# Optimization experiments

Measured on AMD Instinct MI355X. Metric: run time of the kernel, lower is better.

## Reference

```python
import jax, jax.numpy as jnp
import numpy as np

E = 1024   # embed_dim
H = 16     # num_heads
D = E // H # head_dim
B = 2
S = 2048
YAT_EPS = 0.1


def setup_inputs() -> dict:
    key = jax.random.key(0)
    ks = jax.random.split(key, 5)
    w_scale = (6.0 / (E + E)) ** 0.5  # xavier_uniform bound
    def xavier(k):
        return jax.random.uniform(k, (E, E), jnp.float32, -w_scale, w_scale)
    return {
        "x": jax.random.normal(ks[0], (B, S, E), jnp.float32),
        "Wq": xavier(ks[1]), "bq": jnp.zeros((E,), jnp.float32),
        "Wk": xavier(ks[2]), "bk": jnp.zeros((E,), jnp.float32),
        "Wv": xavier(ks[3]), "bv": jnp.zeros((E,), jnp.float32),
        "Wo": xavier(ks[4]), "bo": jnp.zeros((E,), jnp.float32),
    }


def reference(x, Wq, bq, Wk, bk, Wv, bv, Wo, bo):
    b, s, _ = x.shape
    # Projections (Linear: x @ W + b, flax kernel layout [in, out])
    Q = x @ Wq + bq
    K = x @ Wk + bk
    V = x @ Wv + bv
    # [B, H, S, D]
    Q = Q.reshape(b, s, H, D).transpose(0, 2, 1, 3)
    K = K.reshape(b, s, H, D).transpose(0, 2, 1, 3)
    V = V.reshape(b, s, H, D).transpose(0, 2, 1, 3)
    # L2 normalize along head_dim
    Qn = Q / (jnp.linalg.norm(Q, axis=-1, keepdims=True) + 1e-8)
    Kn = K / (jnp.linalg.norm(K, axis=-1, keepdims=True) + 1e-8)
    # Yat kernel scores: (1 + <q,k>)^2 / (eps + (1 - <q,k>))
    dot = jnp.einsum("bhqd,bhkd->bhqk", Qn, Kn)
    scores = (1.0 + dot) ** 2 / (YAT_EPS + (1.0 - dot))
    # Sum-normalize (no softmax)
    attn = scores / (jnp.sum(scores, axis=-1, keepdims=True) + 1e-6)
    out = jnp.einsum("bhqk,bhkd->bhqd", attn, V)
    out = out.transpose(0, 2, 1, 3).reshape(b, s, E)
    return out @ Wo + bo
```

## Files before the change

kernel.cpp:

```cpp
#include <hip/hip_runtime.h>
#include <math.h>

#define EDIM 1024
#define NH   16
#define HD   64
#define BATCH 2
#define SEQ  2048
#define NROW (BATCH*SEQ)
#define YAT_EPS 0.1f

typedef _Float16 f16;
typedef _Float16 f16x8 __attribute__((ext_vector_type(8)));
typedef _Float16 f16x4 __attribute__((ext_vector_type(4)));
typedef float    f32x4 __attribute__((ext_vector_type(4)));

#define GLL16(gp, lp) __builtin_amdgcn_global_load_lds( \
    (const __attribute__((address_space(1))) void*)(gp), \
    (__attribute__((address_space(3))) void*)(lp), 16, 0, 0)

__global__ __launch_bounds__(256)
void cast_f16_kernel(const float* __restrict__ src, f16* __restrict__ dst)
{
    const int i = (blockIdx.x * 256 + threadIdx.x) * 4;
    const float4 v = *(const float4*)(src + i);
    f16x4 o = {(f16)v.x, (f16)v.y, (f16)v.z, (f16)v.w};
    *(f16x4*)(dst + i) = o;
}

__global__ __launch_bounds__(256)
void transcast4_kernel(const float* __restrict__ W0, const float* __restrict__ W1,
                       const float* __restrict__ W2, const float* __restrict__ W3,
                       f16* __restrict__ T0, f16* __restrict__ T1,
                       f16* __restrict__ T2, f16* __restrict__ T3)
{
    const int z = blockIdx.z;
    const float* W = (z == 0) ? W0 : (z == 1) ? W1 : (z == 2) ? W2 : W3;
    f16*         Wt = (z == 0) ? T0 : (z == 1) ? T1 : (z == 2) ? T2 : T3;

    __shared__ float T[32][33];
    const int t = threadIdx.x;
    const int r = t >> 3, c4 = (t & 7) * 4;
    const int bi = blockIdx.x * 32, bj = blockIdx.y * 32;
    const float4 v = *(const float4*)(W + (size_t)(bi + r) * 1024 + bj + c4);
    T[r][c4 + 0] = v.x; T[r][c4 + 1] = v.y; T[r][c4 + 2] = v.z; T[r][c4 + 3] = v.w;
    __syncthreads();
    f16x4 o = {(f16)T[c4 + 0][r], (f16)T[c4 + 1][r], (f16)T[c4 + 2][r], (f16)T[c4 + 3][r]};
    *(f16x4*)(Wt + (size_t)(bj + r) * 1024 + bi + c4) = o;
}

template<int BM>
__global__ __launch_bounds__(256)
void gemm_f16(const f16* __restrict__ A,
              const f16* __restrict__ B0, const f16* __restrict__ B1, const f16* __restrict__ B2,
              const float* __restrict__ bi0, const float* __restrict__ bi1, const float* __restrict__ bi2,
              void* __restrict__ o0, void* __restrict__ o1, void* __restrict__ o2,
              int e0, int e1, int e2)
{
    constexpr int MT   = BM / 32;
    constexpr int LA   = BM / 64;
    constexpr int ABUF = BM * 32;
    constexpr int BBUF = 128 * 32;
    constexpr int STG  = 2 * (ABUF + BBUF) * 2;
    constexpr int EPI  = BM * 128 * 2;
    constexpr int LDSB = STG > EPI ? STG : EPI;
    __shared__ __align__(16) char lds[LDSB];
    f16* As = (f16*)lds;
    f16* Bs = (f16*)lds + 2 * ABUF;

    const int z = blockIdx.z;
    const f16*   Bt   = (z == 0) ? B0  : (z == 1) ? B1  : B2;
    const float* bias = (z == 0) ? bi0 : (z == 1) ? bi1 : bi2;
    void*        Cout = (z == 0) ? o0  : (z == 1) ? o1  : o2;
    const int    epi  = (z == 0) ? e0  : (z == 1) ? e1  : e2;

    const int tid  = threadIdx.x;
    const int lane = tid & 63;
    const int w    = tid >> 6;
    const int cl   = lane & 15;
    const int quad = lane >> 4;
    const int wm = w & 1, wn = w >> 1;
    const int bm = blockIdx.x * BM, bn = blockIdx.y * 128;
    const int wmoff = wm * (MT * 16);

    const int srow = tid >> 2;
    const int sc   = tid & 3;
    const int ssw  = (sc ^ (srow & 3)) * 8;
    const f16* gA = A  + (size_t)(bm + srow) * 1024 + sc * 8;
    const f16* gB = Bt + (size_t)(bn + srow) * 1024 + sc * 8;
    int lAo[LA], lBo[2];
#pragma unroll
    for (int i = 0; i < LA; ++i) lAo[i] = (srow + i * 64) * 32 + ssw;
#pragma unroll
    for (int i = 0; i < 2;  ++i) lBo[i] = (srow + i * 64) * 32 + ssw;

    f32x4 acc[MT][4];
#pragma unroll
    for (int i = 0; i < MT; ++i)
#pragma unroll
        for (int j = 0; j < 4; ++j) acc[i][j] = (f32x4){0.f, 0.f, 0.f, 0.f};

    f16x8 ra[LA], rb[2];

#pragma unroll
    for (int i = 0; i < LA; ++i) ra[i] = *(const f16x8*)(gA + (size_t)i * 64 * 1024);
#pragma unroll
    for (int i = 0; i < 2;  ++i) rb[i] = *(const f16x8*)(gB + (size_t)i * 64 * 1024);
#pragma unroll
    for (int i = 0; i < LA; ++i) *(f16x8*)(As + lAo[i]) = ra[i];
#pragma unroll
    for (int i = 0; i < 2;  ++i) *(f16x8*)(Bs + lBo[i]) = rb[i];
#pragma unroll
    for (int i = 0; i < LA; ++i) ra[i] = *(const f16x8*)(gA + (size_t)i * 64 * 1024 + 32);
#pragma unroll
    for (int i = 0; i < 2;  ++i) rb[i] = *(const f16x8*)(gB + (size_t)i * 64 * 1024 + 32);
    __syncthreads();

    const int fsw = (quad ^ (cl & 3)) * 8;

    for (int it = 0; it < 32; ++it) {
        const int buf = it & 1, nb = buf ^ 1;
        if (it < 31) {
#pragma unroll
            for (int i = 0; i < LA; ++i) *(f16x8*)(As + nb * ABUF + lAo[i]) = ra[i];
#pragma unroll
            for (int i = 0; i < 2;  ++i) *(f16x8*)(Bs + nb * BBUF + lBo[i]) = rb[i];
        }
        if (it < 30) {
            const int kn = (it + 2) * 32;
#pragma unroll
            for (int i = 0; i < LA; ++i) ra[i] = *(const f16x8*)(gA + (size_t)i * 64 * 1024 + kn);
#pragma unroll
            for (int i = 0; i < 2;  ++i) rb[i] = *(const f16x8*)(gB + (size_t)i * 64 * 1024 + kn);
        }
        f16x8 af[MT], bf[4];
#pragma unroll
        for (int mt = 0; mt < MT; ++mt)
            af[mt] = *(const f16x8*)(&As[buf * ABUF + (wmoff + mt * 16 + cl) * 32 + fsw]);
#pragma unroll
        for (int nt = 0; nt < 4; ++nt)
            bf[nt] = *(const f16x8*)(&Bs[buf * BBUF + (wn * 64 + nt * 16 + cl) * 32 + fsw]);
#pragma unroll
        for (int mt = 0; mt < MT; ++mt)
#pragma unroll
            for (int nt = 0; nt < 4; ++nt)
                acc[mt][nt] = __builtin_amdgcn_mfma_f32_16x16x32_f16(af[mt], bf[nt], acc[mt][nt], 0, 0, 0);
        __syncthreads();
    }

    float bcol[4];
#pragma unroll
    for (int nt = 0; nt < 4; ++nt) bcol[nt] = bias[bn + wn * 64 + nt * 16 + cl];
#pragma unroll
    for (int mt = 0; mt < MT; ++mt)
#pragma unroll
        for (int nt = 0; nt < 4; ++nt)
#pragma unroll
            for (int rg = 0; rg < 4; ++rg) acc[mt][nt][rg] += bcol[nt];

    const int b_idx = bm >> 11, sl0 = bm & (SEQ - 1), h0 = bn >> 6;

    if (epi == 0) {
        float* C = (float*)Cout;
#pragma unroll
        for (int mt = 0; mt < MT; ++mt)
#pragma unroll
            for (int rg = 0; rg < 4; ++rg) {
                const int row = bm + wmoff + mt * 16 + quad * 4 + rg;
#pragma unroll
                for (int nt = 0; nt < 4; ++nt)
                    C[(size_t)row * EDIM + bn + wn * 64 + nt * 16 + cl] = acc[mt][nt][rg];
            }
    } else if (epi == 1) {
        f16* C = (f16*)Cout;
        __syncthreads();
        f16* S = (f16*)lds;
#pragma unroll
        for (int mt = 0; mt < MT; ++mt)
#pragma unroll
            for (int rg = 0; rg < 4; ++rg) {
                float ss = 0.f;
#pragma unroll
                for (int nt = 0; nt < 4; ++nt) ss += acc[mt][nt][rg] * acc[mt][nt][rg];
                ss += __shfl_xor(ss, 1); ss += __shfl_xor(ss, 2);
                ss += __shfl_xor(ss, 4); ss += __shfl_xor(ss, 8);
                const float inv = 1.0f / (sqrtf(ss) + 1e-8f);
                const int row = wmoff + mt * 16 + quad * 4 + rg;
#pragma unroll
                for (int nt = 0; nt < 4; ++nt) {
                    const int col = wn * 64 + nt * 16 + cl;
                    S[row * 128 + (((col >> 3) ^ (row & 15)) * 8) + (col & 7)] =
                        (f16)(acc[mt][nt][rg] * inv);
                }
            }
        __syncthreads();
#pragma unroll
        for (int i = 0; i < BM / 16; ++i) {
            const int c = tid + i * 256;
            const int s = c >> 4, gi = c & 15;
            f16x8 v = *(const f16x8*)(&S[s * 128 + ((gi ^ (s & 15)) * 8)]);
            const int head = h0 + (gi >> 3), d8 = (gi & 7) * 8;
            *(f16x8*)(C + ((size_t)(b_idx * NH + head) * SEQ + sl0 + s) * HD + d8) = v;
        }
    } else {
        f16* C = (f16*)Cout;
        __syncthreads();
        f16* S = (f16*)lds;
        constexpr int GM = BM / 8 - 1;
#pragma unroll
        for (int mt = 0; mt < MT; ++mt) {
            const int s0 = wmoff + mt * 16 + quad * 4;
#pragma unroll
            for (int nt = 0; nt < 4; ++nt) {
                const int col = wn * 64 + nt * 16 + cl;
                f16x4 o = {(f16)acc[mt][nt][0], (f16)acc[mt][nt][1],
                           (f16)acc[mt][nt][2], (f16)acc[mt][nt][3]};
                *(f16x4*)(&S[col * BM + (((s0 >> 3) ^ (col & GM)) * 8) + (s0 & 7)]) = o;
            }
        }
        __syncthreads();
        constexpr int GSH = (BM == 128) ? 4 : 3;
#pragma unroll
        for (int i = 0; i < BM / 16; ++i) {
            const int c = tid + i * 256;
            const int col = c >> GSH, gi = c & GM;
            f16x8 v = *(const f16x8*)(&S[col * BM + ((gi ^ (col & GM)) * 8)]);
            const int head = h0 + (col >> 6), d = col & 63;
            *(f16x8*)(C + ((size_t)(b_idx * NH + head) * HD + d) * SEQ + sl0 + gi * 8) = v;
        }
    }
}

__global__ __launch_bounds__(256)
void yat_attn(const f16* __restrict__ Qh, const f16* __restrict__ Kh,
              const f16* __restrict__ Vt, f16* __restrict__ AO)
{
    __shared__ __align__(16) char lds[53248];
    f16* KsB = (f16*)(lds + 20480);
    f16* VsB = (f16*)(lds + 36864);

    const int tid  = threadIdx.x;
    const int lane = tid & 63;
    const int w    = tid >> 6;
    const int cl   = lane & 15;
    const int quad = lane >> 4;
    const int wm = w & 1;
    const int wk = w >> 1;
    const int q0 = blockIdx.x * 128;
    const int bh = blockIdx.y;

    const f16* Qg = Qh + (size_t)bh * SEQ * HD;
    const f16* Kg = Kh + (size_t)bh * SEQ * HD;
    const f16* Vg = Vt + (size_t)bh * HD * SEQ;

    const int g8   = lane >> 3;
    const int scs  = (lane & 7) ^ g8;
    const int qrow = w * 8 + g8;
    const int krow = w * 16 + g8;

    {
        const f16* gQ = Qg + (size_t)(q0 + qrow) * HD + scs * 8;
        f16* lQ = (f16*)lds + w * 512;
#pragma unroll
        for (int it = 0; it < 4; ++it)
            GLL16(gQ + it * 32 * HD, lQ + it * 2048);
    }
    __syncthreads();
    f16x8 qf[4][2];
#pragma unroll
    for (int qt = 0; qt < 4; ++qt)
#pragma unroll
        for (int kb = 0; kb < 2; ++kb)
            qf[qt][kb] = *(const f16x8*)((f16*)lds + (wm * 64 + qt * 16 + cl) * 64 +
                                         ((kb * 4 + quad) ^ (cl & 7)) * 8);
    __syncthreads();

    f16* Pw = (f16*)(lds + w * 5120);

    f32x4 O[4][4];
    float rs[4] = {0.f, 0.f, 0.f, 0.f};
#pragma unroll
    for (int i = 0; i < 4; ++i)
#pragma unroll
        for (int j = 0; j < 4; ++j) O[i][j] = (f32x4){0.f, 0.f, 0.f, 0.f};

    const f16* gK = Kg + (size_t)krow * HD + scs * 8;
    const f16* gV = Vg + (size_t)krow * SEQ + scs * 8;
    f16* lK = KsB + w * 1024;
    f16* lV = VsB + w * 1024;

#pragma unroll
    for (int it = 0; it < 2; ++it) {
        GLL16(gK + (size_t)(it * 8) * HD, lK + it * 512);
        GLL16(gV + (size_t)(it * 8) * SEQ, lV + it * 512);
    }

    for (int t0 = 0; t0 < SEQ; t0 += 64) {
        const int buf = (t0 >> 6) & 1;
        __syncthreads();

        if (t0 + 64 < SEQ) {
            const int nb = buf ^ 1;
#pragma unroll
            for (int it = 0; it < 2; ++it) {
                GLL16(gK + (size_t)(t0 + 64 + it * 8) * HD, lK + nb * 4096 + it * 512);
                GLL16(gV + (size_t)(it * 8) * SEQ + t0 + 64, lV + nb * 4096 + it * 512);
            }
        }

        const f16* Ks = KsB + buf * 4096;
        const f16* Vs = VsB + buf * 4096;

        f32x4 s[2][4];
#pragma unroll
        for (int kt = 0; kt < 2; ++kt)
#pragma unroll
            for (int qt = 0; qt < 4; ++qt) s[kt][qt] = (f32x4){0.f, 0.f, 0.f, 0.f};
#pragma unroll
        for (int kb = 0; kb < 2; ++kb) {
            const int sw = ((kb * 4 + quad) ^ (cl & 7)) * 8;
            f16x8 af0 = *(const f16x8*)(&Ks[(wk * 32 +  0 + cl) * 64 + sw]);
            f16x8 af1 = *(const f16x8*)(&Ks[(wk * 32 + 16 + cl) * 64 + sw]);
#pragma unroll
            for (int qt = 0; qt < 4; ++qt) {
                s[0][qt] = __builtin_amdgcn_mfma_f32_16x16x32_f16(af0, qf[qt][kb], s[0][qt], 0, 0, 0);
                s[1][qt] = __builtin_amdgcn_mfma_f32_16x16x32_f16(af1, qf[qt][kb], s[1][qt], 0, 0, 0);
            }
        }

#pragma unroll
        for (int kt = 0; kt < 2; ++kt)
#pragma unroll
            for (int qt = 0; qt < 4; ++qt) {
                f16x4 pk;
                float psum = 0.f;
#pragma unroll
                for (int rg = 0; rg < 4; ++rg) {
                    const float u = (1.0f + YAT_EPS) - s[kt][qt][rg];
                    const float p = fmaf(4.41f, __builtin_amdgcn_rcpf(u), u - 4.2f);
                    psum += p;
                    pk[rg] = (f16)p;
                }
                rs[qt] += psum;
                *(f16x4*)(&Pw[(qt * 16 + cl) * 40 + kt * 16 + quad * 4]) = pk;
            }

        f16x8 pa[4];
#pragma unroll
        for (int qt = 0; qt < 4; ++qt)
            pa[qt] = *(const f16x8*)(&Pw[(qt * 16 + cl) * 40 + quad * 8]);
#pragma unroll
        for (int dn = 0; dn < 4; ++dn) {
            f16x8 vb = *(const f16x8*)(&Vs[(dn * 16 + cl) * 64 +
                                           ((wk * 4 + quad) ^ (cl & 7)) * 8]);
#pragma unroll
            for (int qt = 0; qt < 4; ++qt)
                O[qt][dn] = __builtin_amdgcn_mfma_f32_16x16x32_f16(pa[qt], vb, O[qt][dn], 0, 0, 0);
        }
    }

    __syncthreads();
    float* rs_s = (float*)lds;
    float* Ox   = (float*)(lds + 20480);

#pragma unroll
    for (int qt = 0; qt < 4; ++qt) {
        float t = rs[qt];
        t += __shfl_xor(t, 16);
        t += __shfl_xor(t, 32);
        if (quad == 0) rs_s[wk * 128 + wm * 64 + qt * 16 + cl] = t;
    }
    if (wk == 1) {
#pragma unroll
        for (int qt = 0; qt < 4; ++qt)
#pragma unroll
            for (int dn = 0; dn < 4; ++dn)
#pragma unroll
                for (int rg = 0; rg < 4; ++rg)
                    Ox[(wm * 64 + qt * 16 + quad * 4 + rg) * 64 + dn * 16 + cl] = O[qt][dn][rg];
    }
    __syncthreads();
    if (wk == 0) {
        const int b = bh >> 4, h = bh & 15;
#pragma unroll
        for (int qt = 0; qt < 4; ++qt)
#pragma unroll
            for (int rg = 0; rg < 4; ++rg) {
                const int ql = wm * 64 + qt * 16 + quad * 4 + rg;
                const float tot = rs_s[ql] + rs_s[128 + ql];
                const float inv = 1.0f / (tot + 1e-6f);
                const size_t rowoff = ((size_t)b * SEQ + q0 + ql) * EDIM + h * 64;
#pragma unroll
                for (int dn = 0; dn < 4; ++dn)
                    AO[rowoff + dn * 16 + cl] =
                        (f16)((O[qt][dn][rg] + Ox[ql * 64 + dn * 16 + cl]) * inv);
            }
    }
}

extern "C" void kernel_launch(void* const* d_in, const int* in_sizes, int n_in,
                              void* d_out, int out_size, void* d_ws, size_t ws_size,
                              hipStream_t stream)
{
    const float* x  = (const float*)d_in[0];
    const float* Wq = (const float*)d_in[1];
    const float* bq = (const float*)d_in[2];
    const float* Wk = (const float*)d_in[3];
    const float* bk = (const float*)d_in[4];
    const float* Wv = (const float*)d_in[5];
    const float* bv = (const float*)d_in[6];
    const float* Wo = (const float*)d_in[7];
    const float* bo = (const float*)d_in[8];

    char* p = (char*)d_ws;
    f16* xb  = (f16*)p;                 p += (size_t)NROW * EDIM * 2;
    f16* Wqt = (f16*)p;                 p += (size_t)EDIM * EDIM * 2;
    f16* Wkt = (f16*)p;                 p += (size_t)EDIM * EDIM * 2;
    f16* Wvt = (f16*)p;                 p += (size_t)EDIM * EDIM * 2;
    f16* Wot = (f16*)p;                 p += (size_t)EDIM * EDIM * 2;
    f16* Qhb = (f16*)p;                 p += (size_t)NROW * EDIM * 2;
    f16* Khb = (f16*)p;                 p += (size_t)NROW * EDIM * 2;
    f16* Vtb = (f16*)p;                 p += (size_t)NROW * EDIM * 2;
    f16* AOb = (f16*)p;                 p += (size_t)NROW * EDIM * 2;

    cast_f16_kernel<<<NROW * EDIM / 1024, 256, 0, stream>>>(x, xb);
    transcast4_kernel<<<dim3(32, 32, 4), 256, 0, stream>>>(Wq, Wk, Wv, Wo,
                                                           Wqt, Wkt, Wvt, Wot);

    gemm_f16<128><<<dim3(NROW / 128, EDIM / 128, 3), 256, 0, stream>>>(
        xb, Wqt, Wkt, Wvt, bq, bk, bv, Qhb, Khb, Vtb, 1, 1, 2);

    yat_attn<<<dim3(SEQ / 128, BATCH * NH), 256, 0, stream>>>(Qhb, Khb, Vtb, AOb);

    gemm_f16<64><<<dim3(NROW / 64, EDIM / 128, 1), 256, 0, stream>>>(
        AOb, Wot, Wot, Wot, bo, bo, bo, d_out, d_out, d_out, 0, 0, 0);
}
```

Before: 209.2 us.

## Fuse x cast into QKV GEMM and restructure attention to 512 threads

Measured after the change: 205.6 us. No clear change (-1.7%).

```diff
diff --git a/kernel.cpp b/kernel.cpp
--- a/kernel.cpp
+++ b/kernel.cpp
@@ -12,19 +12,21 @@
 typedef _Float16 f16;
 typedef _Float16 f16x8 __attribute__((ext_vector_type(8)));
 typedef _Float16 f16x4 __attribute__((ext_vector_type(4)));
+typedef __fp16   h16x2 __attribute__((ext_vector_type(2)));
 typedef float    f32x4 __attribute__((ext_vector_type(4)));
 
-#define GLL16(gp, lp) __builtin_amdgcn_global_load_lds( \
-    (const __attribute__((address_space(1))) void*)(gp), \
-    (__attribute__((address_space(3))) void*)(lp), 16, 0, 0)
-
-__global__ __launch_bounds__(256)
-void cast_f16_kernel(const float* __restrict__ src, f16* __restrict__ dst)
-{
-    const int i = (blockIdx.x * 256 + threadIdx.x) * 4;
-    const float4 v = *(const float4*)(src + i);
-    f16x4 o = {(f16)v.x, (f16)v.y, (f16)v.z, (f16)v.w};
-    *(f16x4*)(dst + i) = o;
+static __device__ __forceinline__ int pk2(float a, float b) {
+    union { h16x2 h; int i; } u;
+    u.h = __builtin_amdgcn_cvt_pkrtz(a, b);
+    return u.i;
+}
+static __device__ __forceinline__ f16x8 cvt_f16x8(float4 a, float4 b) {
+    union { int i[4]; f16x8 h; } u;
+    u.i[0] = pk2(a.x, a.y);
+    u.i[1] = pk2(a.z, a.w);
+    u.i[2] = pk2(b.x, b.y);
+    u.i[3] = pk2(b.z, b.w);
+    return u.h;
 }
 
 __global__ __launch_bounds__(256)
@@ -48,9 +50,9 @@
     *(f16x4*)(Wt + (size_t)(bj + r) * 1024 + bi + c4) = o;
 }
 
-template<int BM>
+template<int BM, bool AF32>
 __global__ __launch_bounds__(256)
-void gemm_f16(const f16* __restrict__ A,
+void gemm_f16(const void* __restrict__ Av,
               const f16* __restrict__ B0, const f16* __restrict__ B1, const f16* __restrict__ B2,
               const float* __restrict__ bi0, const float* __restrict__ bi1, const float* __restrict__ bi2,
               void* __restrict__ o0, void* __restrict__ o1, void* __restrict__ o2,
@@ -85,8 +87,9 @@
     const int srow = tid >> 2;
     const int sc   = tid & 3;
     const int ssw  = (sc ^ (srow & 3)) * 8;
-    const f16* gA = A  + (size_t)(bm + srow) * 1024 + sc * 8;
-    const f16* gB = Bt + (size_t)(bn + srow) * 1024 + sc * 8;
+    const float* gAf = (const float*)Av + (size_t)(bm + srow) * 1024 + sc * 8;
+    const f16*   gAh = (const f16*)Av   + (size_t)(bm + srow) * 1024 + sc * 8;
+    const f16*   gB  = Bt + (size_t)(bn + srow) * 1024 + sc * 8;
     int lAo[LA], lBo[2];
 #pragma unroll
     for (int i = 0; i < LA; ++i) lAo[i] = (srow + i * 64) * 32 + ssw;
@@ -101,8 +104,12 @@
 
     f16x8 ra[LA], rb[2];
 
-#pragma unroll
-    for (int i = 0; i < LA; ++i) ra[i] = *(const f16x8*)(gA + (size_t)i * 64 * 1024);
+#define LOAD_A(i, kn) (AF32 ? cvt_f16x8(*(const float4*)(gAf + (size_t)(i) * 64 * 1024 + (kn)),      \
+                                        *(const float4*)(gAf + (size_t)(i) * 64 * 1024 + (kn) + 4))  \
+                            : *(const f16x8*)(gAh + (size_t)(i) * 64 * 1024 + (kn)))
+
+#pragma unroll
+    for (int i = 0; i < LA; ++i) ra[i] = LOAD_A(i, 0);
 #pragma unroll
     for (int i = 0; i < 2;  ++i) rb[i] = *(const f16x8*)(gB + (size_t)i * 64 * 1024);
 #pragma unroll
@@ -110,7 +117,7 @@
 #pragma unroll
     for (int i = 0; i < 2;  ++i) *(f16x8*)(Bs + lBo[i]) = rb[i];
 #pragma unroll
-    for (int i = 0; i < LA; ++i) ra[i] = *(const f16x8*)(gA + (size_t)i * 64 * 1024 + 32);
+    for (int i = 0; i < LA; ++i) ra[i] = LOAD_A(i, 32);
 #pragma unroll
     for (int i = 0; i < 2;  ++i) rb[i] = *(const f16x8*)(gB + (size_t)i * 64 * 1024 + 32);
     __syncthreads();
@@ -128,7 +135,7 @@
         if (it < 30) {
             const int kn = (it + 2) * 32;
 #pragma unroll
-            for (int i = 0; i < LA; ++i) ra[i] = *(const f16x8*)(gA + (size_t)i * 64 * 1024 + kn);
+            for (int i = 0; i < LA; ++i) ra[i] = LOAD_A(i, kn);
 #pragma unroll
             for (int i = 0; i < 2;  ++i) rb[i] = *(const f16x8*)(gB + (size_t)i * 64 * 1024 + kn);
         }
@@ -146,6 +153,7 @@
                 acc[mt][nt] = __builtin_amdgcn_mfma_f32_16x16x32_f16(af[mt], bf[nt], acc[mt][nt], 0, 0, 0);
         __syncthreads();
     }
+#undef LOAD_A
 
     float bcol[4];
 #pragma unroll
@@ -230,21 +238,22 @@
     }
 }
 
-__global__ __launch_bounds__(256)
+__global__ __launch_bounds__(512, 4)
 void yat_attn(const f16* __restrict__ Qh, const f16* __restrict__ Kh,
               const f16* __restrict__ Vt, f16* __restrict__ AO)
 {
-    __shared__ __align__(16) char lds[53248];
-    f16* KsB = (f16*)(lds + 20480);
-    f16* VsB = (f16*)(lds + 36864);
+    __shared__ __align__(16) char lds[49152];
+    f16* Qs = (f16*)lds;
+    f16* KB = (f16*)(lds + 16384);
+    f16* VB = (f16*)(lds + 32768);
 
     const int tid  = threadIdx.x;
     const int lane = tid & 63;
     const int w    = tid >> 6;
     const int cl   = lane & 15;
     const int quad = lane >> 4;
-    const int wm = w & 1;
-    const int wk = w >> 1;
+    const int wm = w & 3;
+    const int wk = w >> 2;
     const int q0 = blockIdx.x * 128;
     const int bh = blockIdx.y;
 
@@ -252,140 +261,141 @@
     const f16* Kg = Kh + (size_t)bh * SEQ * HD;
     const f16* Vg = Vt + (size_t)bh * HD * SEQ;
 
-    const int g8   = lane >> 3;
-    const int scs  = (lane & 7) ^ g8;
-    const int qrow = w * 8 + g8;
-    const int krow = w * 16 + g8;
-
-    {
-        const f16* gQ = Qg + (size_t)(q0 + qrow) * HD + scs * 8;
-        f16* lQ = (f16*)lds + w * 512;
-#pragma unroll
-        for (int it = 0; it < 4; ++it)
-            GLL16(gQ + it * 32 * HD, lQ + it * 2048);
+    const int rkv = tid >> 3;
+    const int gkv = tid & 7;
+    const f16* gK = Kg + (size_t)rkv * HD + gkv * 8;
+    const f16* gV = Vg + (size_t)rkv * SEQ + gkv * 8;
+    const int lkOff = rkv * 64 + ((gkv ^ (rkv & 7)) * 8);
+
+    f16x8 kr = *(const f16x8*)(gK);
+    f16x8 vr = *(const f16x8*)(gV);
+
+#pragma unroll
+    for (int i = 0; i < 2; ++i) {
+        const int s0 = tid + i * 512;
+        const int row = s0 >> 3, g = s0 & 7;
+        f16x8 v = *(const f16x8*)(Qg + (size_t)(q0 + row) * HD + g * 8);
+        *(f16x8*)(&Qs[row * 64 + ((g ^ (row & 7)) * 8)]) = v;
     }
     __syncthreads();
-    f16x8 qf[4][2];
-#pragma unroll
-    for (int qt = 0; qt < 4; ++qt)
+    f16x8 qf[2][2];
+#pragma unroll
+    for (int qt = 0; qt < 2; ++qt)
 #pragma unroll
         for (int kb = 0; kb < 2; ++kb)
-            qf[qt][kb] = *(const f16x8*)((f16*)lds + (wm * 64 + qt * 16 + cl) * 64 +
-                                         ((kb * 4 + quad) ^ (cl & 7)) * 8);
-    __syncthreads();
-
-    f16* Pw = (f16*)(lds + w * 5120);
-
-    f32x4 O[4][4];
-    float rs[4] = {0.f, 0.f, 0.f, 0.f};
-#pragma unroll
-    for (int i = 0; i < 4; ++i)
+            qf[qt][kb] = *(const f16x8*)(&Qs[(wm * 32 + qt * 16 + cl) * 64 +
+                                             ((kb * 4 + quad) ^ (cl & 7)) * 8]);
+
+    f32x4 O[2][4];
+    float rs[2] = {0.f, 0.f};
+#pragma unroll
+    for (int i = 0; i < 2; ++i)
 #pragma unroll
         for (int j = 0; j < 4; ++j) O[i][j] = (f32x4){0.f, 0.f, 0.f, 0.f};
 
-    const f16* gK = Kg + (size_t)krow * HD + scs * 8;
-    const f16* gV = Vg + (size_t)krow * SEQ + scs * 8;
-    f16* lK = KsB + w * 1024;
-    f16* lV = VsB + w * 1024;
-
-#pragma unroll
-    for (int it = 0; it < 2; ++it) {
-        GLL16(gK + (size_t)(it * 8) * HD, lK + it * 512);
-        GLL16(gV + (size_t)(it * 8) * SEQ, lV + it * 512);
-    }
-
-    for (int t0 = 0; t0 < SEQ; t0 += 64) {
-        const int buf = (t0 >> 6) & 1;
-        __syncthreads();
-
-        if (t0 + 64 < SEQ) {
-            const int nb = buf ^ 1;
-#pragma unroll
-            for (int it = 0; it < 2; ++it) {
-                GLL16(gK + (size_t)(t0 + 64 + it * 8) * HD, lK + nb * 4096 + it * 512);
-                GLL16(gV + (size_t)(it * 8) * SEQ + t0 + 64, lV + nb * 4096 + it * 512);
-            }
-        }
-
-        const f16* Ks = KsB + buf * 4096;
-        const f16* Vs = VsB + buf * 4096;
-
-        f32x4 s[2][4];
+    const int addrA = ((((quad & 1) << 1) * 16) + cl) << 2;
+    const int addrB = addrA + 64;
+
+    for (int t = 0; t < 32; ++t) {
+        const int buf = t & 1;
+        *(f16x8*)(&KB[buf * 4096 + lkOff]) = kr;
+        *(f16x8*)(&VB[buf * 4096 + lkOff]) = vr;
+        if (t < 31) {
+            kr = *(const f16x8*)(gK + (size_t)(t + 1) * 64 * HD);
+            vr = *(const f16x8*)(gV + (t + 1) * 64);
+        }
+        __syncthreads();
+
+        const f16* Ks = KB + buf * 4096;
+        const f16* Vs = VB + buf * 4096;
+
+        f32x4 s[2][2];
 #pragma unroll
         for (int kt = 0; kt < 2; ++kt)
 #pragma unroll
-            for (int qt = 0; qt < 4; ++qt) s[kt][qt] = (f32x4){0.f, 0.f, 0.f, 0.f};
+            for (int qt = 0; qt < 2; ++qt) s[kt][qt] = (f32x4){0.f, 0.f, 0.f, 0.f};
 #pragma unroll
         for (int kb = 0; kb < 2; ++kb) {
             const int sw = ((kb * 4 + quad) ^ (cl & 7)) * 8;
             f16x8 af0 = *(const f16x8*)(&Ks[(wk * 32 +  0 + cl) * 64 + sw]);
             f16x8 af1 = *(const f16x8*)(&Ks[(wk * 32 + 16 + cl) * 64 + sw]);
 #pragma unroll
-            for (int qt = 0; qt < 4; ++qt) {
+            for (int qt = 0; qt < 2; ++qt) {
                 s[0][qt] = __builtin_amdgcn_mfma_f32_16x16x32_f16(af0, qf[qt][kb], s[0][qt], 0, 0, 0);
                 s[1][qt] = __builtin_amdgcn_mfma_f32_16x16x32_f16(af1, qf[qt][kb], s[1][qt], 0, 0, 0);
             }
         }
 
+        int pks[2][2][2];
 #pragma unroll
         for (int kt = 0; kt < 2; ++kt)
 #pragma unroll
-            for (int qt = 0; qt < 4; ++qt) {
-                f16x4 pk;
-                float psum = 0.f;
+            for (int qt = 0; qt < 2; ++qt) {
+                float p[4];
 #pragma unroll
                 for (int rg = 0; rg < 4; ++rg) {
                     const float u = (1.0f + YAT_EPS) - s[kt][qt][rg];
-                    const float p = fmaf(4.41f, __builtin_amdgcn_rcpf(u), u - 4.2f);
-                    psum += p;
-                    pk[rg] = (f16)p;
+                    p[rg] = fmaf(4.41f, __builtin_amdgcn_rcpf(u), u - 4.2f);
+                    rs[qt] += p[rg];
                 }
-                rs[qt] += psum;
-                *(f16x4*)(&Pw[(qt * 16 + cl) * 40 + kt * 16 + quad * 4]) = pk;
-            }
-
-        f16x8 pa[4];
-#pragma unroll
-        for (int qt = 0; qt < 4; ++qt)
-            pa[qt] = *(const f16x8*)(&Pw[(qt * 16 + cl) * 40 + quad * 8]);
+                pks[kt][qt][0] = pk2(p[0], p[1]);
+                pks[kt][qt][1] = pk2(p[2], p[3]);
+            }
+
+        f16x8 pa[2];
+#pragma unroll
+        for (int qt = 0; qt < 2; ++qt) {
+            union { int i[4]; f16x8 h; } u;
+#pragma unroll
+            for (int j = 0; j < 2; ++j) {
+                int a0 = __builtin_amdgcn_ds_bpermute(addrA, pks[0][qt][j]);
+                int a1 = __builtin_amdgcn_ds_bpermute(addrA, pks[1][qt][j]);
+                u.i[j]     = (quad >= 2) ? a1 : a0;
+                int b0 = __builtin_amdgcn_ds_bpermute(addrB, pks[0][qt][j]);
+                int b1 = __builtin_amdgcn_ds_bpermute(addrB, pks[1][qt][j]);
+                u.i[j + 2] = (quad >= 2) ? b1 : b0;
+            }
+            pa[qt] = u.h;
+        }
+
 #pragma unroll
         for (int dn = 0; dn < 4; ++dn) {
             f16x8 vb = *(const f16x8*)(&Vs[(dn * 16 + cl) * 64 +
                                            ((wk * 4 + quad) ^ (cl & 7)) * 8]);
 #pragma unroll
-            for (int qt = 0; qt < 4; ++qt)
+            for (int qt = 0; qt < 2; ++qt)
                 O[qt][dn] = __builtin_amdgcn_mfma_f32_16x16x32_f16(pa[qt], vb, O[qt][dn], 0, 0, 0);
         }
     }
 
     __syncthreads();
     float* rs_s = (float*)lds;
-    float* Ox   = (float*)(lds + 20480);
-
-#pragma unroll
-    for (int qt = 0; qt < 4; ++qt) {
+    float* Ox   = (float*)(lds + 1024);
+
+#pragma unroll
+    for (int qt = 0; qt < 2; ++qt) {
         float t = rs[qt];
         t += __shfl_xor(t, 16);
         t += __shfl_xor(t, 32);
-        if (quad == 0) rs_s[wk * 128 + wm * 64 + qt * 16 + cl] = t;
+        if (quad == 0) rs_s[wk * 128 + wm * 32 + qt * 16 + cl] = t;
     }
     if (wk == 1) {
 #pragma unroll
-        for (int qt = 0; qt < 4; ++qt)
+        for (int qt = 0; qt < 2; ++qt)
 #pragma unroll
             for (int dn = 0; dn < 4; ++dn)
 #pragma unroll
                 for (int rg = 0; rg < 4; ++rg)
-                    Ox[(wm * 64 + qt * 16 + quad * 4 + rg) * 64 + dn * 16 + cl] = O[qt][dn][rg];
+                    Ox[(wm * 32 + qt * 16 + quad * 4 + rg) * 64 + dn * 16 + cl] = O[qt][dn][rg];
     }
     __syncthreads();
     if (wk == 0) {
         const int b = bh >> 4, h = bh & 15;
 #pragma unroll
-        for (int qt = 0; qt < 4; ++qt)
+        for (int qt = 0; qt < 2; ++qt)
 #pragma unroll
             for (int rg = 0; rg < 4; ++rg) {
-                const int ql = wm * 64 + qt * 16 + quad * 4 + rg;
+                const int ql = wm * 32 + qt * 16 + quad * 4 + rg;
                 const float tot = rs_s[ql] + rs_s[128 + ql];
                 const float inv = 1.0f / (tot + 1e-6f);
                 const size_t rowoff = ((size_t)b * SEQ + q0 + ql) * EDIM + h * 64;
@@ -412,7 +422,6 @@
     const float* bo = (const float*)d_in[8];
 
     char* p = (char*)d_ws;
-    f16* xb  = (f16*)p;                 p += (size_t)NROW * EDIM * 2;
     f16* Wqt = (f16*)p;                 p += (size_t)EDIM * EDIM * 2;
     f16* Wkt = (f16*)p;                 p += (size_t)EDIM * EDIM * 2;
     f16* Wvt = (f16*)p;                 p += (size_t)EDIM * EDIM * 2;
@@ -422,15 +431,14 @@
     f16* Vtb = (f16*)p;                 p += (size_t)NROW * EDIM * 2;
     f16* AOb = (f16*)p;                 p += (size_t)NROW * EDIM * 2;
 
-    cast_f16_kernel<<<NROW * EDIM / 1024, 256, 0, stream>>>(x, xb);
     transcast4_kernel<<<dim3(32, 32, 4), 256, 0, stream>>>(Wq, Wk, Wv, Wo,
                                                            Wqt, Wkt, Wvt, Wot);
 
-    gemm_f16<128><<<dim3(NROW / 128, EDIM / 128, 3), 256, 0, stream>>>(
-        xb, Wqt, Wkt, Wvt, bq, bk, bv, Qhb, Khb, Vtb, 1, 1, 2);
-
-    yat_attn<<<dim3(SEQ / 128, BATCH * NH), 256, 0, stream>>>(Qhb, Khb, Vtb, AOb);
-
-    gemm_f16<64><<<dim3(NROW / 64, EDIM / 128, 1), 256, 0, stream>>>(
+    gemm_f16<128, true><<<dim3(NROW / 128, EDIM / 128, 3), 256, 0, stream>>>(
+        x, Wqt, Wkt, Wvt, bq, bk, bv, Qhb, Khb, Vtb, 1, 1, 2);
+
+    yat_attn<<<dim3(SEQ / 128, BATCH * NH), 512, 0, stream>>>(Qhb, Khb, Vtb, AOb);
+
+    gemm_f16<64, false><<<dim3(NROW / 64, EDIM / 128, 1), 256, 0, stream>>>(
         AOb, Wot, Wot, Wot, bo, bo, bo, d_out, d_out, d_out, 0, 0, 0);
 }
```
